# Performance work log

Hardware: AMD Instinct MI355X
Metric: run time of the kernel (lower is better)

## Reference

```python
import jax, jax.numpy as jnp
import numpy as np

D_MODEL = 1024
NUM_HEADS = 16
HEAD_DIM = D_MODEL // NUM_HEADS
HIDDEN = 4096
EPS = 1e-5


def setup_inputs() -> dict:
    key = jax.random.key(0)
    ks = jax.random.split(key, 10)
    s = 0.02
    return {
        "x": jax.random.normal(ks[0], (2, 2048, D_MODEL), dtype=jnp.float32),
        # attention projection weights stored as (in, out): y = x @ W
        "wq": jax.random.normal(ks[1], (D_MODEL, D_MODEL), dtype=jnp.float32) * s,
        "wk": jax.random.normal(ks[2], (D_MODEL, D_MODEL), dtype=jnp.float32) * s,
        "wv": jax.random.normal(ks[3], (D_MODEL, D_MODEL), dtype=jnp.float32) * s,
        "wo": jax.random.normal(ks[4], (D_MODEL, D_MODEL), dtype=jnp.float32) * s,
        # FFN
        "w1": jax.random.normal(ks[5], (D_MODEL, HIDDEN), dtype=jnp.float32) * s,
        "b1": jnp.zeros((HIDDEN,), dtype=jnp.float32),
        "w2": jax.random.normal(ks[6], (HIDDEN, D_MODEL), dtype=jnp.float32) * s,
        "b2": jnp.zeros((D_MODEL,), dtype=jnp.float32),
        # LayerNorms
        "g1": jnp.ones((D_MODEL,), dtype=jnp.float32),
        "be1": jnp.zeros((D_MODEL,), dtype=jnp.float32),
        "g2": jnp.ones((D_MODEL,), dtype=jnp.float32),
        "be2": jnp.zeros((D_MODEL,), dtype=jnp.float32),
    }


def _layernorm(x, g, b):
    mu = jnp.mean(x, axis=-1, keepdims=True)
    var = jnp.mean(jnp.square(x - mu), axis=-1, keepdims=True)
    return (x - mu) * jax.lax.rsqrt(var + EPS) * g + b


def _attention(x, wq, wk, wv, wo):
    B, S, D = x.shape
    q = (x @ wq).reshape(B, S, NUM_HEADS, HEAD_DIM)
    k = (x @ wk).reshape(B, S, NUM_HEADS, HEAD_DIM)
    v = (x @ wv).reshape(B, S, NUM_HEADS, HEAD_DIM)
    scores = jnp.einsum("bqhd,bkhd->bhqk", q, k) / jnp.sqrt(
        jnp.float32(HEAD_DIM)
    )
    causal = jnp.tril(jnp.ones((S, S), dtype=bool))
    scores = jnp.where(causal, scores, -jnp.inf)
    probs = jax.nn.softmax(scores, axis=-1)
    out = jnp.einsum("bhqk,bkhd->bqhd", probs, v).reshape(B, S, D)
    return out @ wo


def _ffn(x, w1, b1, w2, b2):
    return jax.nn.relu(x @ w1 + b1) @ w2 + b2


def reference(x, wq, wk, wv, wo, w1, b1, w2, b2, g1, be1, g2, be2):
    x = x + _attention(_layernorm(x, g1, be1), wq, wk, wv, wo)
    x = x + _ffn(_layernorm(x, g2, be2), w1, b1, w2, b2)
    return x
```

## Files before the change

### kernel.cpp

```cpp
#include <hip/hip_runtime.h>
#include <stdint.h>

typedef unsigned short bf16u;
typedef __attribute__((ext_vector_type(8))) __bf16 bf16x8;
typedef __attribute__((ext_vector_type(4))) float f32x4;
typedef __attribute__((ext_vector_type(4))) unsigned short u16x4;

typedef __attribute__((address_space(1))) void gvoid_t;
typedef __attribute__((address_space(3))) void lvoid_t;

#define SEQ 2048
#define DM 1024

__device__ __forceinline__ bf16u f2bf(float f) {
  union { float f; uint32_t u; } v; v.f = f;
  uint32_t u = v.u + 0x7fffu + ((v.u >> 16) & 1u);
  return (bf16u)(u >> 16);
}

__device__ __forceinline__ void async_copy16(const bf16u* g, const bf16u* l) {
  __builtin_amdgcn_global_load_lds((gvoid_t*)(uintptr_t)g,
                                   (lvoid_t*)(uint32_t)(uintptr_t)l,
                                   16, 0, 0);
}

#define VM_WAIT(n) asm volatile("s_waitcnt vmcnt(" #n ")" ::: "memory")
#define LGKM0()    asm volatile("s_waitcnt lgkmcnt(0)" ::: "memory")
#define BARRIER()  asm volatile("s_barrier" ::: "memory")

__global__ __launch_bounds__(256) void ln_kernel(const float* __restrict__ x,
                                                 const float* __restrict__ g,
                                                 const float* __restrict__ be,
                                                 bf16u* __restrict__ out) {
  const int row = blockIdx.x;
  const int t = threadIdx.x;
  const float4 v = ((const float4*)(x + (size_t)row * DM))[t];
  float s  = v.x + v.y + v.z + v.w;
  float ss = v.x * v.x + v.y * v.y + v.z * v.z + v.w * v.w;
#pragma unroll
  for (int m = 1; m < 64; m <<= 1) {
    s  += __shfl_xor(s, m, 64);
    ss += __shfl_xor(ss, m, 64);
  }
  __shared__ float red[2][4];
  const int wv = t >> 6, ln = t & 63;
  if (ln == 0) { red[0][wv] = s; red[1][wv] = ss; }
  __syncthreads();
  s  = red[0][0] + red[0][1] + red[0][2] + red[0][3];
  ss = red[1][0] + red[1][1] + red[1][2] + red[1][3];
  const float mu = s * (1.0f / DM);
  const float var = ss * (1.0f / DM) - mu * mu;
  const float rstd = rsqrtf(var + 1e-5f);
  const float4 gg = ((const float4*)g)[t];
  const float4 bb = ((const float4*)be)[t];
  u16x4 o;
  o[0] = f2bf((v.x - mu) * rstd * gg.x + bb.x);
  o[1] = f2bf((v.y - mu) * rstd * gg.y + bb.y);
  o[2] = f2bf((v.z - mu) * rstd * gg.z + bb.z);
  o[3] = f2bf((v.w - mu) * rstd * gg.w + bb.w);
  *(u16x4*)(out + (size_t)row * DM + t * 4) = o;
}

__global__ __launch_bounds__(256) void wtrans(const float* __restrict__ in,
                                              bf16u* __restrict__ out, int R, int C) {
  __shared__ float tile[32][33];
  const int c0 = blockIdx.x * 32, r0 = blockIdx.y * 32;
  const int tx = threadIdx.x, ty = threadIdx.y;
#pragma unroll
  for (int i = 0; i < 4; ++i)
    tile[ty + i * 8][tx] = in[(size_t)(r0 + ty + i * 8) * C + c0 + tx];
  __syncthreads();
#pragma unroll
  for (int i = 0; i < 4; ++i)
    out[(size_t)(c0 + ty + i * 8) * R + r0 + tx] = f2bf(tile[tx][ty + i * 8]);
}

__global__ __launch_bounds__(256) void wtrans4(const float* __restrict__ a,
                                               const float* __restrict__ b,
                                               const float* __restrict__ c,
                                               const float* __restrict__ d,
                                               bf16u* __restrict__ out) {
  const float* srcs[4] = {a, b, c, d};
  const float* in = srcs[blockIdx.z];
  bf16u* o = out + (size_t)blockIdx.z * 1024 * 1024;
  __shared__ float tile[32][33];
  const int c0 = blockIdx.x * 32, r0 = blockIdx.y * 32;
  const int tx = threadIdx.x, ty = threadIdx.y;
#pragma unroll
  for (int i = 0; i < 4; ++i)
    tile[ty + i * 8][tx] = in[(size_t)(r0 + ty + i * 8) * 1024 + c0 + tx];
  __syncthreads();
#pragma unroll
  for (int i = 0; i < 4; ++i)
    o[(size_t)(c0 + ty + i * 8) * 1024 + r0 + tx] = f2bf(tile[tx][ty + i * 8]);
}

__global__ __launch_bounds__(256) void vtrans(const bf16u* __restrict__ qkv,
                                              bf16u* __restrict__ vt) {
  __shared__ bf16u tile[32][33];
  const int s0 = blockIdx.x * 32;
  const int d0 = blockIdx.y * 32;
  const int bh = blockIdx.z, b = bh >> 4, h = bh & 15;
  const int tx = threadIdx.x, ty = threadIdx.y;
#pragma unroll
  for (int i = 0; i < 4; ++i)
    tile[ty + i * 8][tx] =
        qkv[(size_t)(b * SEQ + s0 + ty + i * 8) * 3072 + 2048 + h * 64 + d0 + tx];
  __syncthreads();
#pragma unroll
  for (int i = 0; i < 4; ++i)
    vt[(size_t)(bh * 64 + d0 + ty + i * 8) * SEQ + s0 + tx] = tile[tx][ty + i * 8];
}

__global__ __launch_bounds__(512, 1) void gemm256(
    const bf16u* __restrict__ A, const bf16u* __restrict__ Bt,
    int M, int N, int K,
    const float* __restrict__ bias, bf16u* __restrict__ outB,
    float* __restrict__ outF, int mode, int lgS) {
  __shared__ bf16u sh[2][32768];
  const int t = threadIdx.x;
  const int ln = t & 63;
  const int wv = t >> 6;
  const int col16 = ln & 15, quad = ln >> 4;
  const int wm = wv >> 2, wn = wv & 3;

  const int nbx = N >> 8;
  const int nwg = (nbx * (M >> 8)) << lgS;
  const int cpx = nwg >> 3;
  const int bid = blockIdx.x;
  const int swz = (bid & 7) * cpx + (bid >> 3);
  const int split = swz & ((1 << lgS) - 1);
  const int tile = swz >> lgS;
  const int m0 = (tile / nbx) << 8, n0 = (tile % nbx) << 8;
  const int Ks = K >> lgS;
  const size_t koff = (size_t)split * Ks;

  const bf16u* gsrc[4][2];
  int doff[4][2];
#pragma unroll
  for (int j = 0; j < 2; ++j) {
    const int c = t + (j << 9);
    const int lr = c >> 3, slot = (c & 7) ^ (lr & 7);
    const int ra = (lr & 63) + ((lr >> 6) << 7);
    const int rb = (lr & 31) + ((lr >> 5) << 6);
    gsrc[0][j] = A  + (size_t)(m0 + ra) * K + koff + slot * 8;
    gsrc[3][j] = A  + (size_t)(m0 + ra + 64) * K + koff + slot * 8;
    gsrc[1][j] = Bt + (size_t)(n0 + rb) * K + koff + slot * 8;
    gsrc[2][j] = Bt + (size_t)(n0 + rb + 32) * K + koff + slot * 8;
    doff[0][j] = c * 8;
    doff[3][j] = 8192 + c * 8;
    doff[1][j] = 16384 + c * 8;
    doff[2][j] = 24576 + c * 8;
  }

  const int sx = col16 & 7;
  int aoffs[4][2], boffs[2][2];
#pragma unroll
  for (int i = 0; i < 4; ++i)
#pragma unroll
    for (int kc = 0; kc < 2; ++kc)
      aoffs[i][kc] = (wm * 64 + i * 16 + col16) * 64 + (((kc << 2) + quad) ^ sx) * 8;
#pragma unroll
  for (int i = 0; i < 2; ++i)
#pragma unroll
    for (int kc = 0; kc < 2; ++kc)
      boffs[i][kc] = 16384 + (wn * 32 + i * 16 + col16) * 64 + (((kc << 2) + quad) ^ sx) * 8;

  f32x4 acc[8][4] = {};
  bf16x8 Af[4][2], Bf[4][2];

  auto stage = [&](int s, int b) {
#pragma unroll
    for (int j = 0; j < 2; ++j) {
      async_copy16(gsrc[s][j], &sh[b][doff[s][j]]);
      gsrc[s][j] += 64;
    }
  };
  auto readA = [&](int b, int mh) {
#pragma unroll
    for (int i = 0; i < 4; ++i)
#pragma unroll
      for (int kc = 0; kc < 2; ++kc)
        Af[i][kc] = *(const bf16x8*)(&sh[b][mh * 8192 + aoffs[i][kc]]);
  };
  auto readB = [&](int b, int nh) {
#pragma unroll
    for (int i = 0; i < 2; ++i)
#pragma unroll
      for (int kc = 0; kc < 2; ++kc)
        Bf[nh * 2 + i][kc] = *(const bf16x8*)(&sh[b][nh * 8192 + boffs[i][kc]]);
  };
  auto mfmaQ = [&](int mh, int nh) {
#pragma unroll
    for (int kc = 0; kc < 2; ++kc)
#pragma unroll
      for (int mi = 0; mi < 4; ++mi)
#pragma unroll
        for (int nl = 0; nl < 2; ++nl)
          acc[mh * 4 + mi][nh * 2 + nl] = __builtin_amdgcn_mfma_f32_16x16x32_bf16(
              Af[mi][kc], Bf[nh * 2 + nl][kc], acc[mh * 4 + mi][nh * 2 + nl], 0, 0, 0);
  };

  const int nt = Ks >> 6;
  stage(0, 0); stage(1, 0); stage(2, 0); stage(3, 0);
  VM_WAIT(4);
  BARRIER();

  int bsel = 0;
  for (int kt = 0; kt < nt - 1; ++kt, bsel ^= 1) {
    const int bn = bsel ^ 1;
    readA(bsel, 0); readB(bsel, 0);
    stage(0, bn);
    BARRIER(); LGKM0();
    __builtin_amdgcn_s_setprio(1); mfmaQ(0, 0); __builtin_amdgcn_s_setprio(0);
    VM_WAIT(4); BARRIER();
    readB(bsel, 1);
    stage(1, bn);
    BARRIER(); LGKM0();
    __builtin_amdgcn_s_setprio(1); mfmaQ(0, 1); __builtin_amdgcn_s_setprio(0);
    VM_WAIT(4); BARRIER();
    readA(bsel, 1);
    stage(2, bn);
    BARRIER(); LGKM0();
    __builtin_amdgcn_s_setprio(1); mfmaQ(1, 0); __builtin_amdgcn_s_setprio(0);
    BARRIER();
    stage(3, bn);
    __builtin_amdgcn_s_setprio(1); mfmaQ(1, 1); __builtin_amdgcn_s_setprio(0);
    VM_WAIT(4); BARRIER();
  }
  readA(bsel, 0); readB(bsel, 0);
  BARRIER(); LGKM0();
  __builtin_amdgcn_s_setprio(1); mfmaQ(0, 0); __builtin_amdgcn_s_setprio(0);
  VM_WAIT(2); BARRIER();
  readB(bsel, 1);
  BARRIER(); LGKM0();
  __builtin_amdgcn_s_setprio(1); mfmaQ(0, 1); __builtin_amdgcn_s_setprio(0);
  VM_WAIT(0); BARRIER();
  readA(bsel, 1);
  LGKM0();
  __builtin_amdgcn_s_setprio(1); mfmaQ(1, 0); mfmaQ(1, 1); __builtin_amdgcn_s_setprio(0);

  if (mode == 4) {
    float bv[4] = {0.f, 0.f, 0.f, 0.f};
    if (split == 0 && bias) {
#pragma unroll
      for (int n = 0; n < 4; ++n) bv[n] = bias[n0 + wn * 64 + n * 16 + col16];
    }
#pragma unroll
    for (int mi = 0; mi < 8; ++mi) {
#pragma unroll
      for (int n = 0; n < 4; ++n) {
        const int col = n0 + wn * 64 + n * 16 + col16;
#pragma unroll
        for (int r = 0; r < 4; ++r) {
          const int row = m0 + wm * 128 + mi * 16 + quad * 4 + r;
          unsafeAtomicAdd(&outF[(size_t)row * N + col], acc[mi][n][r] + bv[n]);
        }
      }
    }
    return;
  }
  float bv[4];
  if (mode == 1) {
#pragma unroll
    for (int n = 0; n < 4; ++n) bv[n] = bias[n0 + wn * 64 + n * 16 + col16];
  }
#pragma unroll
  for (int mi = 0; mi < 8; ++mi) {
#pragma unroll
    for (int n = 0; n < 4; ++n) {
      const int col = n0 + wn * 64 + n * 16 + col16;
#pragma unroll
      for (int r = 0; r < 4; ++r) {
        const int row = m0 + wm * 128 + mi * 16 + quad * 4 + r;
        float v = acc[mi][n][r];
        if (mode == 1) v = fmaxf(v + bv[n], 0.0f);
        outB[(size_t)row * N + col] = f2bf(v);
      }
    }
  }
}

__global__ __launch_bounds__(256, 3) void gemm_bt64(
    const bf16u* __restrict__ A, const bf16u* __restrict__ Bt,
    int M, int N, int K,
    const float* __restrict__ bias, const float* __restrict__ resid,
    bf16u* __restrict__ outB, float* __restrict__ outF, int mode) {
  __shared__ bf16u As0[64 * 64], As1[64 * 64];
  __shared__ bf16u Bs0[128 * 64], Bs1[128 * 64];
  const int t = threadIdx.x;
  const int ln = t & 63;
  const int wv = t >> 6;
  const int col16 = ln & 15, quad = ln >> 4;

  const int nbx = gridDim.x;
  const int nwg = nbx * gridDim.y;
  const int cpx = nwg >> 3;
  const int flat = blockIdx.y * nbx + blockIdx.x;
  const int swz = (flat & 7) * cpx + (flat >> 3);
  const int m0 = (swz / nbx) * 64, n0 = (swz % nbx) * 128;

  const bf16u* gA[2];
  const bf16u* gB[4];
#pragma unroll
  for (int j = 0; j < 2; ++j) {
    const int c = t + 256 * j, row = c >> 3, slot = (c & 7) ^ (row & 7);
    gA[j] = A + (size_t)(m0 + row) * K + slot * 8;
  }
#pragma unroll
  for (int j = 0; j < 4; ++j) {
    const int c = t + 256 * j, row = c >> 3, slot = (c & 7) ^ (row & 7);
    gB[j] = Bt + (size_t)(n0 + row) * K + slot * 8;
  }

  f32x4 acc[4][2] = {};

  auto stage = [&](bf16u* dA, bf16u* dB) {
#pragma unroll
    for (int j = 0; j < 2; ++j) {
      async_copy16(gA[j], dA + (size_t)(t + 256 * j) * 8);
      gA[j] += 64;
    }
#pragma unroll
    for (int j = 0; j < 4; ++j) {
      async_copy16(gB[j], dB + (size_t)(t + 256 * j) * 8);
      gB[j] += 64;
    }
  };
  auto compute = [&](const bf16u* sA, const bf16u* sB) {
    bf16x8 af[4][2], bfv[2][2];
#pragma unroll
    for (int mi = 0; mi < 4; ++mi) {
      const int row = mi * 16 + col16;
#pragma unroll
      for (int kc = 0; kc < 2; ++kc)
        af[mi][kc] = *(const bf16x8*)(sA + row * 64 + (((kc << 2) + quad) ^ (row & 7)) * 8);
    }
#pragma unroll
    for (int ni = 0; ni < 2; ++ni) {
      const int row = wv * 32 + ni * 16 + col16;
#pragma unroll
      for (int kc = 0; kc < 2; ++kc)
        bfv[ni][kc] = *(const bf16x8*)(sB + row * 64 + (((kc << 2) + quad) ^ (row & 7)) * 8);
    }
#pragma unroll
    for (int kc = 0; kc < 2; ++kc)
#pragma unroll
      for (int mi = 0; mi < 4; ++mi)
#pragma unroll
        for (int ni = 0; ni < 2; ++ni)
          acc[mi][ni] = __builtin_amdgcn_mfma_f32_16x16x32_bf16(af[mi][kc], bfv[ni][kc],
                                                                acc[mi][ni], 0, 0, 0);
  };

  const int niter = K >> 6;
  stage(As0, Bs0);
  for (int k = 0; k < niter; k += 2) {
    stage(As1, Bs1);
    VM_WAIT(6);
    BARRIER();
    compute(As0, Bs0);
    BARRIER();
    if (k + 2 < niter) {
      stage(As0, Bs0);
      VM_WAIT(6);
    } else {
      VM_WAIT(0);
    }
    BARRIER();
    compute(As1, Bs1);
    BARRIER();
  }

#pragma unroll
  for (int mi = 0; mi < 4; ++mi) {
#pragma unroll
    for (int ni = 0; ni < 2; ++ni) {
      const int col = n0 + wv * 32 + ni * 16 + col16;
#pragma unroll
      for (int r = 0; r < 4; ++r) {
        const int row = m0 + mi * 16 + quad * 4 + r;
        float v = acc[mi][ni][r];
        if (mode == 1 || mode == 3) v += bias[col];
        if (mode == 1) v = fmaxf(v, 0.0f);
        if (mode >= 2) {
          outF[(size_t)row * N + col] = v + resid[(size_t)row * N + col];
        } else {
          outB[(size_t)row * N + col] = f2bf(v);
        }
      }
    }
  }
}

#define PST 132
#define SCL 0.18033688f
__global__ __launch_bounds__(256, 3) void attn_kernel(const bf16u* __restrict__ qkv,
                                                      const bf16u* __restrict__ vt,
                                                      bf16u* __restrict__ out) {
  __shared__ bf16u Ks[128 * 64];
  __shared__ bf16u Vts[2 * 64 * 64];
  __shared__ bf16u pbuf[4][16 * PST];
  __shared__ float lred[4][16];
  const int t = threadIdx.x;
  const int wv = t >> 6, ln = t & 63;
  const int col = ln & 15, quad = ln >> 4;
  const int bh = blockIdx.x, b = bh >> 4, h = bh & 15;
  const int strip = 31 - blockIdx.y;
  const int q0 = strip * 64;
  const int qw = q0 + wv * 16;
  const int qmax = qw + 15;
  const int ntiles = (q0 >> 7) + 1;

  int krow[4], kslot[4], vrow[4], vsub[4], vslot[4];
  const bf16u *kl[4], *vl[4];
#pragma unroll
  for (int j = 0; j < 4; ++j) {
    const int c = t + 256 * j;
    krow[j] = c >> 3; kslot[j] = (c & 7) ^ (krow[j] & 7);
    const int rem = c & 511;
    vsub[j] = c >> 9; vrow[j] = rem >> 3; vslot[j] = (rem & 7) ^ (vrow[j] & 7);
    kl[j] = Ks + (size_t)c * 8;
    vl[j] = Vts + (size_t)c * 8;
  }

  bf16x8 qf0, qf1;
  {
    const size_t qoff = (size_t)(b * SEQ + qw + col) * 3072 + h * 64 + quad * 8;
    qf0 = *(const bf16x8*)(qkv + qoff);
    qf1 = *(const bf16x8*)(qkv + qoff + 32);
  }
  f32x4 po[4] = {};
  float ll[4] = {};

  for (int kb = 0; kb < ntiles; ++kb) {
    const int kbase = kb * 128;
#pragma unroll
    for (int j = 0; j < 4; ++j) {
      async_copy16(qkv + (size_t)(b * SEQ + kbase + krow[j]) * 3072 + 1024 + h * 64 + kslot[j] * 8, kl[j]);
      async_copy16(vt + (size_t)(bh * 64 + vrow[j]) * SEQ + kbase + vsub[j] * 64 + vslot[j] * 8, vl[j]);
    }
    asm volatile("s_waitcnt vmcnt(0)" ::: "memory");
    __syncthreads();

    if (kb < ntiles - 1) {
      f32x4 sc[8];
#pragma unroll
      for (int n = 0; n < 8; ++n) {
        const int kr = n * 16 + col;
        const bf16x8 k0 = *(const bf16x8*)(Ks + kr * 64 + (quad ^ (kr & 7)) * 8);
        const bf16x8 k1 = *(const bf16x8*)(Ks + kr * 64 + ((4 + quad) ^ (kr & 7)) * 8);
        f32x4 z = {};
        z = __builtin_amdgcn_mfma_f32_16x16x32_bf16(qf0, k0, z, 0, 0, 0);
        sc[n] = __builtin_amdgcn_mfma_f32_16x16x32_bf16(qf1, k1, z, 0, 0, 0);
      }
#pragma unroll
      for (int r = 0; r < 4; ++r) {
#pragma unroll
        for (int n = 0; n < 8; ++n) {
          const float e = exp2f(sc[n][r] * SCL);
          ll[r] += e;
          pbuf[wv][(quad * 4 + r) * PST + n * 16 + col] = f2bf(e);
        }
      }
    } else {
      f32x4 sc[8];
      bool act[8];
#pragma unroll
      for (int n = 0; n < 8; ++n) {
        act[n] = (kbase + n * 16) <= qmax;
        if (act[n]) {
          const int kr = n * 16 + col;
          const bf16x8 k0 = *(const bf16x8*)(Ks + kr * 64 + (quad ^ (kr & 7)) * 8);
          const bf16x8 k1 = *(const bf16x8*)(Ks + kr * 64 + ((4 + quad) ^ (kr & 7)) * 8);
          f32x4 z = {};
          z = __builtin_amdgcn_mfma_f32_16x16x32_bf16(qf0, k0, z, 0, 0, 0);
          sc[n] = __builtin_amdgcn_mfma_f32_16x16x32_bf16(qf1, k1, z, 0, 0, 0);
        }
      }
#pragma unroll
      for (int r = 0; r < 4; ++r) {
        const int q = qw + quad * 4 + r;
#pragma unroll
        for (int n = 0; n < 8; ++n) {
          float e = 0.0f;
          if (act[n]) {
            float v = sc[n][r] * SCL;
            v = (kbase + n * 16 + col <= q) ? v : -1e30f;
            e = exp2f(v);
          }
          ll[r] += e;
          pbuf[wv][(quad * 4 + r) * PST + n * 16 + col] = f2bf(e);
        }
      }
    }
    asm volatile("s_waitcnt lgkmcnt(0)" ::: "memory");
    bf16x8 pa[4];
#pragma unroll
    for (int kc = 0; kc < 4; ++kc)
      pa[kc] = *(const bf16x8*)(&pbuf[wv][col * PST + kc * 32 + quad * 8]);
    if (kb < ntiles - 1) {
#pragma unroll
      for (int n = 0; n < 4; ++n) {
        const int vr = n * 16 + col;
#pragma unroll
        for (int kc = 0; kc < 4; ++kc) {
          const bf16x8 vfr = *(const bf16x8*)(Vts + (kc >> 1) * 4096 + vr * 64 +
                                              (((kc & 1) * 4 + quad) ^ (vr & 7)) * 8);
          po[n] = __builtin_amdgcn_mfma_f32_16x16x32_bf16(vfr, pa[kc], po[n], 0, 0, 0);
        }
      }
    } else {
#pragma unroll
      for (int n = 0; n < 4; ++n) {
        const int vr = n * 16 + col;
#pragma unroll
        for (int kc = 0; kc < 4; ++kc)
          if (kbase + kc * 32 <= qmax) {
            const bf16x8 vfr = *(const bf16x8*)(Vts + (kc >> 1) * 4096 + vr * 64 +
                                                (((kc & 1) * 4 + quad) ^ (vr & 7)) * 8);
            po[n] = __builtin_amdgcn_mfma_f32_16x16x32_bf16(vfr, pa[kc], po[n], 0, 0, 0);
          }
      }
    }
    asm volatile("s_waitcnt lgkmcnt(0)" ::: "memory");
    __syncthreads();
  }

#pragma unroll
  for (int m = 1; m < 16; m <<= 1)
#pragma unroll
    for (int r = 0; r < 4; ++r) ll[r] += __shfl_xor(ll[r], m, 64);
  if (col == 0) {
#pragma unroll
    for (int r = 0; r < 4; ++r) lred[wv][quad * 4 + r] = ll[r];
  }
  asm volatile("s_waitcnt lgkmcnt(0)" ::: "memory");
  const float inv = 1.0f / lred[wv][col];
#pragma unroll
  for (int n = 0; n < 4; ++n) {
    u16x4 o;
#pragma unroll
    for (int r = 0; r < 4; ++r) o[r] = f2bf(po[n][r] * inv);
    *(u16x4*)(out + (size_t)(b * SEQ + qw + col) * DM + h * 64 + n * 16 + quad * 4) = o;
  }
}

extern "C" void kernel_launch(void* const* d_in, const int* in_sizes, int n_in,
                              void* d_out, int out_size, void* d_ws, size_t ws_size,
                              hipStream_t stream) {
  const float* x   = (const float*)d_in[0];
  const float* wq  = (const float*)d_in[1];
  const float* wk  = (const float*)d_in[2];
  const float* wvv = (const float*)d_in[3];
  const float* wo  = (const float*)d_in[4];
  const float* w1  = (const float*)d_in[5];
  const float* b1  = (const float*)d_in[6];
  const float* w2  = (const float*)d_in[7];
  const float* b2  = (const float*)d_in[8];
  const float* g1  = (const float*)d_in[9];
  const float* be1 = (const float*)d_in[10];
  const float* g2  = (const float*)d_in[11];
  const float* be2 = (const float*)d_in[12];
  float* out = (float*)d_out;

  char* ws = (char*)d_ws;
  bf16u* wqkv_t = (bf16u*)(ws);
  bf16u* wo_t   = (bf16u*)(ws +  6291456);
  bf16u* w1_t   = (bf16u*)(ws +  8388608);
  bf16u* w2_t   = (bf16u*)(ws + 16777216);
  bf16u* lnbuf  = (bf16u*)(ws + 25165824);
  bf16u* qkv    = (bf16u*)(ws + 33554432);
  bf16u* vtb    = (bf16u*)(ws + 58720256);
  bf16u* h1     = (bf16u*)(ws + 33554432);
  bf16u* attn   = lnbuf;

  const dim3 tb32(32, 8);
  wtrans4<<<dim3(32, 32, 4), tb32, 0, stream>>>(wq, wk, wvv, wo, wqkv_t);
  wtrans<<<dim3(128, 32), tb32, 0, stream>>>(w1, w1_t, 1024, 4096);
  wtrans<<<dim3(32, 128), tb32, 0, stream>>>(w2, w2_t, 4096, 1024);

  ln_kernel<<<4096, 256, 0, stream>>>(x, g1, be1, lnbuf);
  gemm256<<<192, 512, 0, stream>>>(lnbuf, wqkv_t, 4096, 3072, 1024,
                                   nullptr, qkv, nullptr, 0, 0);
  vtrans<<<dim3(64, 2, 32), tb32, 0, stream>>>(qkv, vtb);
  attn_kernel<<<dim3(32, 32), 256, 0, stream>>>(qkv, vtb, attn);
  gemm_bt64<<<dim3(8, 64), 256, 0, stream>>>(attn, wo_t, 4096, 1024, 1024,
                                             nullptr, x, nullptr, out, 2);
  ln_kernel<<<4096, 256, 0, stream>>>(out, g2, be2, lnbuf);
  gemm256<<<256, 512, 0, stream>>>(lnbuf, w1_t, 4096, 4096, 1024,
                                   b1, h1, nullptr, 1, 0);
  gemm256<<<256, 512, 0, stream>>>(h1, w2_t, 4096, 1024, 4096,
                                   b2, nullptr, out, 4, 2);
}
```

Before: 353.8 us.

## Fuse V transpose into QKV GEMM epilogue and replace split-K atomics with partial-buffer reduction

The QKV GEMM now writes the V third directly in transposed per-head layout, so the separate vtrans kernel is no longer needed. The FFN down-projection moves from a 4-way split-K with fp32 atomic adds to a 3-way split-K over 192 workgroups. Each split writes bf16 partials to workspace, and a new elementwise reduce3 kernel sums them with bias and residual. This removes atomic traffic and one launch, but adds an extra kernel and rounds partial sums to bf16. It also reuses the weight-transpose and lnbuf workspace regions for the partials.

New measurement: 324.0 us. 8.4% less time.

```diff
diff --git a/kernel.cpp b/kernel.cpp
--- a/kernel.cpp
+++ b/kernel.cpp
@@ -5,17 +5,23 @@
 typedef __attribute__((ext_vector_type(8))) __bf16 bf16x8;
 typedef __attribute__((ext_vector_type(4))) float f32x4;
 typedef __attribute__((ext_vector_type(4))) unsigned short u16x4;
+typedef __attribute__((ext_vector_type(8))) unsigned short u16x8;
 
 typedef __attribute__((address_space(1))) void gvoid_t;
 typedef __attribute__((address_space(3))) void lvoid_t;
 
 #define SEQ 2048
 #define DM 1024
+#define MN22 4194304
 
 __device__ __forceinline__ bf16u f2bf(float f) {
   union { float f; uint32_t u; } v; v.f = f;
   uint32_t u = v.u + 0x7fffu + ((v.u >> 16) & 1u);
   return (bf16u)(u >> 16);
+}
+
+__device__ __forceinline__ float bf2f(bf16u b) {
+  union { uint32_t u; float f; } v; v.u = (uint32_t)b << 16; return v.f;
 }
 
 __device__ __forceinline__ void async_copy16(const bf16u* g, const bf16u* l) {
@@ -95,28 +101,36 @@
     o[(size_t)(c0 + ty + i * 8) * 1024 + r0 + tx] = f2bf(tile[tx][ty + i * 8]);
 }
 
-__global__ __launch_bounds__(256) void vtrans(const bf16u* __restrict__ qkv,
-                                              bf16u* __restrict__ vt) {
-  __shared__ bf16u tile[32][33];
-  const int s0 = blockIdx.x * 32;
-  const int d0 = blockIdx.y * 32;
-  const int bh = blockIdx.z, b = bh >> 4, h = bh & 15;
-  const int tx = threadIdx.x, ty = threadIdx.y;
-#pragma unroll
-  for (int i = 0; i < 4; ++i)
-    tile[ty + i * 8][tx] =
-        qkv[(size_t)(b * SEQ + s0 + ty + i * 8) * 3072 + 2048 + h * 64 + d0 + tx];
-  __syncthreads();
-#pragma unroll
-  for (int i = 0; i < 4; ++i)
-    vt[(size_t)(bh * 64 + d0 + ty + i * 8) * SEQ + s0 + tx] = tile[tx][ty + i * 8];
+__global__ __launch_bounds__(256) void reduce3(const bf16u* __restrict__ p01,
+                                               const bf16u* __restrict__ p2,
+                                               const float* __restrict__ bias,
+                                               float* __restrict__ out) {
+  const size_t i8 = ((size_t)blockIdx.x * 256 + threadIdx.x) * 8;
+  const int col0 = (int)(i8 & 1023);
+  const u16x8 a = *(const u16x8*)(p01 + i8);
+  const u16x8 b = *(const u16x8*)(p01 + MN22 + i8);
+  const u16x8 c = *(const u16x8*)(p2 + i8);
+  const float4 o0 = *(const float4*)(out + i8);
+  const float4 o1 = *(const float4*)(out + i8 + 4);
+  const float4 b0 = *(const float4*)(bias + col0);
+  const float4 b1 = *(const float4*)(bias + col0 + 4);
+  float r[8];
+#pragma unroll
+  for (int j = 0; j < 8; ++j) r[j] = bf2f(a[j]) + bf2f(b[j]) + bf2f(c[j]);
+  float4 w0, w1;
+  w0.x = o0.x + r[0] + b0.x; w0.y = o0.y + r[1] + b0.y;
+  w0.z = o0.z + r[2] + b0.z; w0.w = o0.w + r[3] + b0.w;
+  w1.x = o1.x + r[4] + b1.x; w1.y = o1.y + r[5] + b1.y;
+  w1.z = o1.z + r[6] + b1.z; w1.w = o1.w + r[7] + b1.w;
+  *(float4*)(out + i8) = w0;
+  *(float4*)(out + i8 + 4) = w1;
 }
 
 __global__ __launch_bounds__(512, 1) void gemm256(
     const bf16u* __restrict__ A, const bf16u* __restrict__ Bt,
     int M, int N, int K,
     const float* __restrict__ bias, bf16u* __restrict__ outB,
-    float* __restrict__ outF, int mode, int lgS) {
+    bf16u* __restrict__ vt, int mode) {
   __shared__ bf16u sh[2][32768];
   const int t = threadIdx.x;
   const int ln = t & 63;
@@ -124,16 +138,18 @@
   const int col16 = ln & 15, quad = ln >> 4;
   const int wm = wv >> 2, wn = wv & 3;
 
+  const int nsplit = (mode == 6) ? 3 : 1;
   const int nbx = N >> 8;
-  const int nwg = (nbx * (M >> 8)) << lgS;
+  const int nwg = nbx * (M >> 8) * nsplit;
   const int cpx = nwg >> 3;
   const int bid = blockIdx.x;
   const int swz = (bid & 7) * cpx + (bid >> 3);
-  const int split = swz & ((1 << lgS) - 1);
-  const int tile = swz >> lgS;
+  const int tile = swz / nsplit, split = swz - tile * nsplit;
   const int m0 = (tile / nbx) << 8, n0 = (tile % nbx) << 8;
-  const int Ks = K >> lgS;
-  const size_t koff = (size_t)split * Ks;
+  const int tsteps = K >> 6;
+  const int kbeg = (split * tsteps) / nsplit;
+  const int nt = ((split + 1) * tsteps) / nsplit - kbeg;
+  const size_t koff = (size_t)kbeg << 6;
 
   const bf16u* gsrc[4][2];
   int doff[4][2];
@@ -201,7 +217,6 @@
               Af[mi][kc], Bf[nh * 2 + nl][kc], acc[mh * 4 + mi][nh * 2 + nl], 0, 0, 0);
   };
 
-  const int nt = Ks >> 6;
   stage(0, 0); stage(1, 0); stage(2, 0); stage(3, 0);
   VM_WAIT(4);
   BARRIER();
@@ -240,12 +255,8 @@
   LGKM0();
   __builtin_amdgcn_s_setprio(1); mfmaQ(1, 0); mfmaQ(1, 1); __builtin_amdgcn_s_setprio(0);
 
-  if (mode == 4) {
-    float bv[4] = {0.f, 0.f, 0.f, 0.f};
-    if (split == 0 && bias) {
-#pragma unroll
-      for (int n = 0; n < 4; ++n) bv[n] = bias[n0 + wn * 64 + n * 16 + col16];
-    }
+  if (mode == 6) {
+    bf16u* pb = (split < 2) ? outB + (size_t)split * MN22 : vt;
 #pragma unroll
     for (int mi = 0; mi < 8; ++mi) {
 #pragma unroll
@@ -254,8 +265,25 @@
 #pragma unroll
         for (int r = 0; r < 4; ++r) {
           const int row = m0 + wm * 128 + mi * 16 + quad * 4 + r;
-          unsafeAtomicAdd(&outF[(size_t)row * N + col], acc[mi][n][r] + bv[n]);
+          pb[(size_t)row * N + col] = f2bf(acc[mi][n][r]);
         }
+      }
+    }
+    return;
+  }
+  if (mode == 5 && n0 >= 2048) {
+#pragma unroll
+    for (int mi = 0; mi < 8; ++mi) {
+#pragma unroll
+      for (int n = 0; n < 4; ++n) {
+        const int col = n0 + wn * 64 + n * 16 + col16;
+        const int hh = (col - 2048) >> 6, d = (col - 2048) & 63;
+        const int row_base = m0 + wm * 128 + mi * 16 + quad * 4;
+        const int bb = row_base >> 11, s = row_base & 2047;
+        u16x4 o;
+#pragma unroll
+        for (int r = 0; r < 4; ++r) o[r] = f2bf(acc[mi][n][r]);
+        *(u16x4*)(vt + (size_t)((bb * 16 + hh) * 64 + d) * SEQ + s) = o;
       }
     }
     return;
@@ -574,6 +602,8 @@
   bf16u* vtb    = (bf16u*)(ws + 58720256);
   bf16u* h1     = (bf16u*)(ws + 33554432);
   bf16u* attn   = lnbuf;
+  bf16u* p01 = (bf16u*)(ws);
+  bf16u* p2  = (bf16u*)(ws + 25165824);
 
   const dim3 tb32(32, 8);
   wtrans4<<<dim3(32, 32, 4), tb32, 0, stream>>>(wq, wk, wvv, wo, wqkv_t);
@@ -582,14 +612,14 @@
 
   ln_kernel<<<4096, 256, 0, stream>>>(x, g1, be1, lnbuf);
   gemm256<<<192, 512, 0, stream>>>(lnbuf, wqkv_t, 4096, 3072, 1024,
-                                   nullptr, qkv, nullptr, 0, 0);
-  vtrans<<<dim3(64, 2, 32), tb32, 0, stream>>>(qkv, vtb);
+                                   nullptr, qkv, vtb, 5);
   attn_kernel<<<dim3(32, 32), 256, 0, stream>>>(qkv, vtb, attn);
   gemm_bt64<<<dim3(8, 64), 256, 0, stream>>>(attn, wo_t, 4096, 1024, 1024,
                                              nullptr, x, nullptr, out, 2);
   ln_kernel<<<4096, 256, 0, stream>>>(out, g2, be2, lnbuf);
   gemm256<<<256, 512, 0, stream>>>(lnbuf, w1_t, 4096, 4096, 1024,
-                                   b1, h1, nullptr, 1, 0);
-  gemm256<<<256, 512, 0, stream>>>(h1, w2_t, 4096, 1024, 4096,
-                                   b2, nullptr, out, 4, 2);
-}
+                                   b1, h1, nullptr, 1);
+  gemm256<<<192, 512, 0, stream>>>(h1, w2_t, 4096, 1024, 4096,
+                                   nullptr, p01, p2, 6);
+  reduce3<<<2048, 256, 0, stream>>>(p01, p2, b2, out);
+}
```
